# Optimization experiments

Measured on AMD Instinct MI355X. Metric: run time of the kernel, lower is better.

## Reference

```python
import jax, jax.numpy as jnp
import numpy as np

D_MODEL = 1024
N_HEAD = 16
D_HEAD = D_MODEL // N_HEAD
N_EXPERTS = 8
TOP_K = 2
D_FF = 4096
EPS = 1e-6


def setup_inputs() -> dict:
    key = jax.random.key(0)
    ks = jax.random.split(key, 16)
    s = 0.02  # init scale
    d, dff, E = D_MODEL, D_FF, N_EXPERTS
    return {
        "dec": jax.random.normal(ks[0], (4, 1024, d), jnp.float32),
        "text_encoder": jax.random.normal(ks[1], (4, 512, d), jnp.float32),
        # self-attention projections
        "Wq1": jax.random.normal(ks[2], (d, d), jnp.float32) * s,
        "Wk1": jax.random.normal(ks[3], (d, d), jnp.float32) * s,
        "Wv1": jax.random.normal(ks[4], (d, d), jnp.float32) * s,
        "Wo1": jax.random.normal(ks[5], (d, d), jnp.float32) * s,
        # cross-attention projections
        "Wq2": jax.random.normal(ks[6], (d, d), jnp.float32) * s,
        "Wk2": jax.random.normal(ks[7], (d, d), jnp.float32) * s,
        "Wv2": jax.random.normal(ks[8], (d, d), jnp.float32) * s,
        "Wo2": jax.random.normal(ks[9], (d, d), jnp.float32) * s,
        # shared RMSNorm gain (module uses one norm instance three times)
        "g": jnp.ones((d,), jnp.float32),
        # MoE router + per-expert FFN weights
        "Wg": jax.random.normal(ks[10], (d, E), jnp.float32) * s,
        "W1": jax.random.normal(ks[11], (E, d, dff), jnp.float32) * s,
        "W2": jax.random.normal(ks[12], (E, dff, d), jnp.float32) * s,
    }


def rmsnorm(x, g):
    return x * jax.lax.rsqrt(jnp.mean(x * x, axis=-1, keepdims=True) + EPS) * g


def mha(q_in, k_in, v_in, Wq, Wk, Wv, Wo):
    B, Sq, _ = q_in.shape
    Sk = k_in.shape[1]
    q = (q_in @ Wq).reshape(B, Sq, N_HEAD, D_HEAD)
    k = (k_in @ Wk).reshape(B, Sk, N_HEAD, D_HEAD)
    v = (v_in @ Wv).reshape(B, Sk, N_HEAD, D_HEAD)
    scores = jnp.einsum("bqhd,bkhd->bhqk", q, k) / jnp.sqrt(jnp.asarray(D_HEAD, q.dtype))
    attn = jax.nn.softmax(scores, axis=-1)
    out = jnp.einsum("bhqk,bkhd->bqhd", attn, v).reshape(B, Sq, D_MODEL)
    return out @ Wo


def moe(x, Wg, W1, W2):
    # top-k softmax router, renormalized weights; dense per-expert FFN with combine
    probs = jax.nn.softmax(x @ Wg, axis=-1)              # [B,S,E]
    weights, indices = jax.lax.top_k(probs, TOP_K)        # [B,S,k]
    weights = weights / jnp.sum(weights, axis=-1, keepdims=True)
    # combine[t,e] = sum_k weights[t,k] * (indices[t,k]==e)
    combine = jnp.sum(
        jax.nn.one_hot(indices, N_EXPERTS, dtype=x.dtype) * weights[..., None], axis=-2
    )  # [B,S,E]
    out = jnp.zeros_like(x)
    for e in range(N_EXPERTS):  # fixed small expert loop
        h = jax.nn.relu(x @ W1[e]) @ W2[e]
        out = out + combine[..., e:e + 1] * h
    return weights, indices, out


def reference(dec, text_encoder, Wq1, Wk1, Wv1, Wo1, Wq2, Wk2, Wv2, Wo2, g, Wg, W1, W2):
    # self-attention + residual + RMSNorm (dropout p=0 -> identity)
    x = rmsnorm(mha(dec, dec, dec, Wq1, Wk1, Wv1, Wo1) + dec, g)
    # cross-attention + residual + RMSNorm
    x = rmsnorm(mha(x, text_encoder, text_encoder, Wq2, Wk2, Wv2, Wo2) + x, g)
    # MoE FFN + residual + RMSNorm
    weights, indices, y = moe(x, Wg, W1, W2)
    x = rmsnorm(y + x, g)
    return weights, indices, x
```

## Files before the change

kernel.cpp:

```cpp
#include <hip/hip_runtime.h>
#include <stdint.h>

#define D_    1024
#define BB    4
#define SDEC  1024
#define STXT  512
#define TDEC  4096
#define TTXT  2048
#define NH    16
#define DHD   64
#define NE    8
#define DFF   4096
#define NSLOT 8192
#define ND1   8192
#define ND2   4096
#define MOEGRID 512

using u16 = unsigned short;
typedef __attribute__((ext_vector_type(8))) short bf16x8;
typedef __attribute__((ext_vector_type(4))) float f32x4;

__device__ __forceinline__ float bf2f(u16 h) {
    union { unsigned int u; float f; } x; x.u = ((unsigned int)h) << 16; return x.f;
}
__device__ __forceinline__ u16 f2bf(float f) {
    union { float f; unsigned int u; } x; x.f = f;
    unsigned int lsb = (x.u >> 16) & 1u;
    return (u16)((x.u + 0x7fffu + lsb) >> 16);
}

__device__ __forceinline__ void gld16(const u16* g, u16* l) {
    __builtin_amdgcn_global_load_lds((const __attribute__((address_space(1))) void*)g,
                                     (__attribute__((address_space(3))) void*)l,
                                     16, 0, 0);
}

constexpr int BM = 128, BK = 32;

template<int SPLIT, int EPI, int BROWS>
__global__ __launch_bounds__(256) void gemm_bt(
    const u16* __restrict__ AH, const u16* __restrict__ AL,
    const u16* __restrict__ BH, const u16* __restrict__ BL,
    float* __restrict__ Cf, u16* __restrict__ CH, u16* __restrict__ CL,
    int M, int N, int K, int lda, int ldb, int ldc, int nb2,
    long strA1, long strA2, long strB1, long strB2, long strC1, long strC2)
{
    constexpr int WM = (BROWS == 64) ? 2 : 4;
    constexpr int ASZ = BM * BK, BSZ = BROWS * BK;
    __shared__ u16 smem[(SPLIT ? 2 : 1) * (ASZ + BSZ)];
    u16* sAH = smem;
    u16* sBH = smem + ASZ;
    u16* sAL = SPLIT ? smem + ASZ + BSZ : nullptr;
    u16* sBL = SPLIT ? smem + 2 * ASZ + BSZ : nullptr;

    const int z = blockIdx.z;
    const int z1 = z / nb2, z2 = z % nb2;
    const long zA = (long)z1 * strA1 + (long)z2 * strA2;
    const long zB = (long)z1 * strB1 + (long)z2 * strB2;
    const long zC = (long)z1 * strC1 + (long)z2 * strC2;

    const int tileM = blockIdx.y * BM, tileN = blockIdx.x * BROWS;
    const int t = threadIdx.x;
    const int sr = t >> 2;
    const int sc = (t & 3) << 3;
    const u16* pA = AH + zA + (long)(tileM + sr) * lda + sc;
    const u16* pB = BH + zB + (long)(tileN + sr) * ldb + sc;
    const u16* pAl = nullptr; const u16* pBl = nullptr;
    if constexpr (SPLIT) {
        pAl = AL + zA + (long)(tileM + sr) * lda + sc;
        pBl = BL + zB + (long)(tileN + sr) * ldb + sc;
    }
    const long hA = 64L * lda, hB = 64L * ldb;

    const int lane = t & 63;
    const int wv = t >> 6;
    const int wr = (BROWS == 64) ? (wv << 5) : ((wv >> 1) << 6);
    const int wc = (BROWS == 64) ? 0 : ((wv & 1) << 6);
    const int fr = lane & 15, kg = lane >> 4;

    f32x4 acc[WM][4];
    const f32x4 vzero = {0.f, 0.f, 0.f, 0.f};
#pragma unroll
    for (int m = 0; m < WM; ++m)
#pragma unroll
        for (int n = 0; n < 4; ++n) acc[m][n] = vzero;

    for (int k0 = 0; k0 < K; k0 += BK) {
        gld16(pA + k0,      sAH + t * 8);
        gld16(pA + k0 + hA, sAH + 2048 + t * 8);
        gld16(pB + k0,      sBH + t * 8);
        if constexpr (BROWS == 128) gld16(pB + k0 + hB, sBH + 2048 + t * 8);
        if constexpr (SPLIT) {
            gld16(pAl + k0,      sAL + t * 8);
            gld16(pAl + k0 + hA, sAL + 2048 + t * 8);
            gld16(pBl + k0,      sBL + t * 8);
            if constexpr (BROWS == 128) gld16(pBl + k0 + hB, sBL + 2048 + t * 8);
        }
        __syncthreads();

        bf16x8 fa[WM], fb[4], fal[WM], fbl[4];
#pragma unroll
        for (int m = 0; m < WM; ++m) {
            fa[m] = *(const bf16x8*)&sAH[(wr + m * 16 + fr) * BK + (kg << 3)];
            if constexpr (SPLIT) fal[m] = *(const bf16x8*)&sAL[(wr + m * 16 + fr) * BK + (kg << 3)];
        }
#pragma unroll
        for (int n = 0; n < 4; ++n) {
            fb[n] = *(const bf16x8*)&sBH[(wc + n * 16 + fr) * BK + (kg << 3)];
            if constexpr (SPLIT) fbl[n] = *(const bf16x8*)&sBL[(wc + n * 16 + fr) * BK + (kg << 3)];
        }
#pragma unroll
        for (int m = 0; m < WM; ++m)
#pragma unroll
            for (int n = 0; n < 4; ++n) {
                acc[m][n] = __builtin_amdgcn_mfma_f32_16x16x32_bf16(fa[m], fb[n], acc[m][n], 0, 0, 0);
                if constexpr (SPLIT) {
                    acc[m][n] = __builtin_amdgcn_mfma_f32_16x16x32_bf16(fa[m],  fbl[n], acc[m][n], 0, 0, 0);
                    acc[m][n] = __builtin_amdgcn_mfma_f32_16x16x32_bf16(fal[m], fb[n],  acc[m][n], 0, 0, 0);
                }
            }
        __syncthreads();
    }

#pragma unroll
    for (int m = 0; m < WM; ++m) {
        const int r0 = tileM + wr + m * 16 + (kg << 2);
#pragma unroll
        for (int n = 0; n < 4; ++n) {
            const int col = tileN + wc + n * 16 + fr;
            if (col >= N) continue;
#pragma unroll
            for (int i = 0; i < 4; ++i) {
                const int r = r0 + i;
                if (r >= M) continue;
                const float v = acc[m][n][i];
                const long off = zC + (long)r * ldc + col;
                if constexpr (EPI == 0) {
                    Cf[off] = v;
                } else if constexpr (EPI == 1) {
                    const u16 h = f2bf(v);
                    CH[off] = h;
                    CL[off] = f2bf(v - bf2f(h));
                } else {
                    CH[off] = f2bf(fmaxf(v, 0.f));
                }
            }
        }
    }
}

__global__ __launch_bounds__(256) void scores_k64(
    const u16* __restrict__ AH, const u16* __restrict__ AL,
    const u16* __restrict__ BH, const u16* __restrict__ BL,
    u16* __restrict__ CH, u16* __restrict__ CL,
    int lda, int ldb, int ldc, int nb2,
    long strA1, long strA2, long strB1, long strB2, long strC1, long strC2)
{
    __shared__ u16 smem[4 * 8192];
    u16* sAH = smem;
    u16* sAL = smem + 8192;
    u16* sBH = smem + 16384;
    u16* sBL = smem + 24576;

    const int z = blockIdx.z;
    const int z1 = z / nb2, z2 = z % nb2;
    const long zA = (long)z1 * strA1 + (long)z2 * strA2;
    const long zB = (long)z1 * strB1 + (long)z2 * strB2;
    const long zC = (long)z1 * strC1 + (long)z2 * strC2;

    const int tileM = blockIdx.y * 128, tileN = blockIdx.x * 128;
    const int t = threadIdx.x;
    const int srow = t >> 3;
    const int scol = ((t & 7) ^ (srow & 7)) << 3;
    const u16* pA  = AH + zA + (long)(tileM + srow) * lda + scol;
    const u16* pAl = AL + zA + (long)(tileM + srow) * lda + scol;
    const u16* pB  = BH + zB + (long)(tileN + srow) * ldb + scol;
    const u16* pBl = BL + zB + (long)(tileN + srow) * ldb + scol;

#pragma unroll
    for (int c = 0; c < 4; ++c) {
        const long ro = 32L * c * lda;
        const long rb = 32L * c * ldb;
        gld16(pA  + ro, sAH + c * 2048 + t * 8);
        gld16(pAl + ro, sAL + c * 2048 + t * 8);
        gld16(pB  + rb, sBH + c * 2048 + t * 8);
        gld16(pBl + rb, sBL + c * 2048 + t * 8);
    }
    __syncthreads();

    const int lane = t & 63;
    const int wv = t >> 6;
    const int wr = (wv >> 1) << 6, wc = (wv & 1) << 6;
    const int fr = lane & 15, kg = lane >> 4;

    f32x4 acc[4][4];
    const f32x4 vzero = {0.f, 0.f, 0.f, 0.f};
#pragma unroll
    for (int m = 0; m < 4; ++m)
#pragma unroll
        for (int n = 0; n < 4; ++n) acc[m][n] = vzero;

#pragma unroll
    for (int ks = 0; ks < 2; ++ks) {
        bf16x8 fa[4], fb[4], fal[4], fbl[4];
#pragma unroll
        for (int m = 0; m < 4; ++m) {
            const int r = wr + m * 16 + fr;
            const int o = r * 64 + (((kg | (ks << 2)) ^ (r & 7)) << 3);
            fa[m]  = *(const bf16x8*)&sAH[o];
            fal[m] = *(const bf16x8*)&sAL[o];
        }
#pragma unroll
        for (int n = 0; n < 4; ++n) {
            const int r = wc + n * 16 + fr;
            const int o = r * 64 + (((kg | (ks << 2)) ^ (r & 7)) << 3);
            fb[n]  = *(const bf16x8*)&sBH[o];
            fbl[n] = *(const bf16x8*)&sBL[o];
        }
#pragma unroll
        for (int m = 0; m < 4; ++m)
#pragma unroll
            for (int n = 0; n < 4; ++n) {
                acc[m][n] = __builtin_amdgcn_mfma_f32_16x16x32_bf16(fa[m],  fb[n],  acc[m][n], 0, 0, 0);
                acc[m][n] = __builtin_amdgcn_mfma_f32_16x16x32_bf16(fa[m],  fbl[n], acc[m][n], 0, 0, 0);
                acc[m][n] = __builtin_amdgcn_mfma_f32_16x16x32_bf16(fal[m], fb[n],  acc[m][n], 0, 0, 0);
            }
    }

#pragma unroll
    for (int m = 0; m < 4; ++m) {
        const int r0 = tileM + wr + m * 16 + (kg << 2);
#pragma unroll
        for (int n = 0; n < 4; ++n) {
            const int col = tileN + wc + n * 16 + fr;
#pragma unroll
            for (int i = 0; i < 4; ++i) {
                const float v = acc[m][n][i];
                const long off = zC + (long)(r0 + i) * ldc + col;
                const u16 h = f2bf(v);
                CH[off] = h;
                CL[off] = f2bf(v - bf2f(h));
            }
        }
    }
}

__global__ __launch_bounds__(256) void pv_k64(
    const u16* __restrict__ PHp, const u16* __restrict__ PLp,
    const u16* __restrict__ VTH, const u16* __restrict__ VTL,
    float* __restrict__ Op, int Skv, int NZ)
{
    __shared__ u16 smem[24576];
    u16* sAH = smem;
    u16* sAL = smem + 8192;
    u16* sBH = smem + 16384;
    u16* sBL = smem + 20480;

    const int kq = blockIdx.x;
    const int tileM = blockIdx.y * 128;
    const int z = blockIdx.z;
    const int kbase = kq * (Skv >> 2);
    const int nrounds = Skv >> 8;

    const int t = threadIdx.x;
    const int srow = t >> 3;
    const int scol = ((t & 7) ^ (srow & 7)) << 3;
    const u16* pA  = PHp + (long)z * 1024 * Skv + (long)(tileM + srow) * Skv + kbase + scol;
    const u16* pAl = PLp + (long)z * 1024 * Skv + (long)(tileM + srow) * Skv + kbase + scol;
    const u16* pB  = VTH + (long)z * 64 * Skv + (long)srow * Skv + kbase + scol;
    const u16* pBl = VTL + (long)z * 64 * Skv + (long)srow * Skv + kbase + scol;

    const int lane = t & 63, wv = t >> 6;
    const int wr = wv << 5;
    const int fr = lane & 15, kg = lane >> 4;

    f32x4 acc[2][4];
    const f32x4 vzero = {0.f, 0.f, 0.f, 0.f};
#pragma unroll
    for (int m = 0; m < 2; ++m)
#pragma unroll
        for (int n = 0; n < 4; ++n) acc[m][n] = vzero;

    for (int rr = 0; rr < nrounds; ++rr) {
        const long k0 = (long)rr << 6;
#pragma unroll
        for (int c = 0; c < 4; ++c) {
            const long ro = 32L * c * Skv;
            gld16(pA  + k0 + ro, sAH + c * 2048 + t * 8);
            gld16(pAl + k0 + ro, sAL + c * 2048 + t * 8);
        }
#pragma unroll
        for (int c = 0; c < 2; ++c) {
            const long ro = 32L * c * Skv;
            gld16(pB  + k0 + ro, sBH + c * 2048 + t * 8);
            gld16(pBl + k0 + ro, sBL + c * 2048 + t * 8);
        }
        __syncthreads();

#pragma unroll
        for (int ks = 0; ks < 2; ++ks) {
            bf16x8 fa[2], fb[4], fal[2], fbl[4];
#pragma unroll
            for (int m = 0; m < 2; ++m) {
                const int r = wr + m * 16 + fr;
                const int o = r * 64 + (((kg | (ks << 2)) ^ (r & 7)) << 3);
                fa[m]  = *(const bf16x8*)&sAH[o];
                fal[m] = *(const bf16x8*)&sAL[o];
            }
#pragma unroll
            for (int n = 0; n < 4; ++n) {
                const int r = n * 16 + fr;
                const int o = r * 64 + (((kg | (ks << 2)) ^ (r & 7)) << 3);
                fb[n]  = *(const bf16x8*)&sBH[o];
                fbl[n] = *(const bf16x8*)&sBL[o];
            }
#pragma unroll
            for (int m = 0; m < 2; ++m)
#pragma unroll
                for (int n = 0; n < 4; ++n) {
                    acc[m][n] = __builtin_amdgcn_mfma_f32_16x16x32_bf16(fa[m],  fb[n],  acc[m][n], 0, 0, 0);
                    acc[m][n] = __builtin_amdgcn_mfma_f32_16x16x32_bf16(fa[m],  fbl[n], acc[m][n], 0, 0, 0);
                    acc[m][n] = __builtin_amdgcn_mfma_f32_16x16x32_bf16(fal[m], fb[n],  acc[m][n], 0, 0, 0);
                }
        }
        __syncthreads();
    }

    const long base = ((long)kq * NZ + z) * 65536;
#pragma unroll
    for (int m = 0; m < 2; ++m) {
        const int r0 = tileM + wr + m * 16 + (kg << 2);
#pragma unroll
        for (int n = 0; n < 4; ++n) {
            const int col = n * 16 + fr;
#pragma unroll
            for (int i = 0; i < 4; ++i)
                Op[base + (long)(r0 + i) * 64 + col] = acc[m][n][i];
        }
    }
}

__global__ __launch_bounds__(256) void pv_combine(
    const float* __restrict__ Op, u16* __restrict__ aoH, u16* __restrict__ aoL,
    int nz, int nh)
{
    const long i = ((long)blockIdx.x * 256 + threadIdx.x) * 4;
    const int zz = (int)(i >> 16);
    const int rem = (int)(i & 65535);
    const int r = rem >> 6, c = rem & 63;
    const int b = zz / nh, h = zz % nh;
    const long kqS = (long)nz * 65536;
    float4 v = *(const float4*)(Op + i);
    const float4 v1 = *(const float4*)(Op + kqS + i);
    const float4 v2 = *(const float4*)(Op + 2 * kqS + i);
    const float4 v3 = *(const float4*)(Op + 3 * kqS + i);
    v.x += v1.x + v2.x + v3.x;
    v.y += v1.y + v2.y + v3.y;
    v.z += v1.z + v2.z + v3.z;
    v.w += v1.w + v2.w + v3.w;
    const long dst = (long)b * SDEC * D_ + (long)r * D_ + h * 64 + c;
    u16 h0 = f2bf(v.x), h1 = f2bf(v.y), h2 = f2bf(v.z), h3 = f2bf(v.w);
    uint2 hh;
    hh.x = (unsigned)h0 | ((unsigned)h1 << 16);
    hh.y = (unsigned)h2 | ((unsigned)h3 << 16);
    *(uint2*)(aoH + dst) = hh;
    u16 l0 = f2bf(v.x - bf2f(h0)), l1 = f2bf(v.y - bf2f(h1));
    u16 l2 = f2bf(v.z - bf2f(h2)), l3 = f2bf(v.w - bf2f(h3));
    uint2 ll;
    ll.x = (unsigned)l0 | ((unsigned)l1 << 16);
    ll.y = (unsigned)l2 | ((unsigned)l3 << 16);
    *(uint2*)(aoL + dst) = ll;
}

template<int EPI>
__global__ __launch_bounds__(256, 2) void moe_gemm2(
    const u16* __restrict__ Ag, int lda,
    const u16* __restrict__ BTbase, int ldb, long btStride,
    float* __restrict__ Cf0, float* __restrict__ Cf1, u16* __restrict__ CH, int ldc,
    const int4* __restrict__ desc, int ndesc, int Kiter)
{
    __shared__ u16 smem[32768];
    const int t = threadIdx.x;
    const int lane = t & 63, wv = t >> 6;
    const int wr = (wv >> 1) << 6, wc = (wv & 1) << 6;
    const int fr = lane & 15, kg = lane >> 4;
    const int nks = Kiter >> 5;

    const int rS = t >> 2;
    const int cS = ((t & 3) ^ ((t >> 3) & 3)) << 3;

    int ldsA[4], ldsB[4];
#pragma unroll
    for (int m = 0; m < 4; ++m) {
        const int ra = wr + m * 16 + fr;
        ldsA[m] = ra * 32 + ((kg ^ ((ra >> 1) & 3)) << 3);
        const int rb = wc + m * 16 + fr;
        ldsB[m] = rb * 32 + ((kg ^ ((rb >> 1) & 3)) << 3);
    }

    for (int p = blockIdx.x; p < ndesc; p += MOEGRID) {
        const int4 d = desc[p];
        if (d.x < 0) continue;
        const int rowbase = d.x, colbase = d.y & 0xFFFF, e = d.y >> 16;
        const int kbase = d.z, s1 = d.w;
        const u16* paS = Ag + (long)(rowbase + rS) * lda + kbase + cS;
        const u16* pbS = BTbase + (long)e * btStride + (long)(colbase + rS) * ldb + kbase + cS;
        const long hA = 64L * lda, hB = 64L * ldb;

        f32x4 acc[4][4];
        const f32x4 vzero = {0.f, 0.f, 0.f, 0.f};
#pragma unroll
        for (int m = 0; m < 4; ++m)
#pragma unroll
            for (int n = 0; n < 4; ++n) acc[m][n] = vzero;

#define STG(ks) { const int s_ = (ks) & 3; const long k0_ = (long)(ks) << 5; \
        u16* b_ = smem + s_ * 8192; \
        gld16(paS + k0_,      b_ + t * 8); \
        gld16(paS + k0_ + hA, b_ + 2048 + t * 8); \
        gld16(pbS + k0_,      b_ + 4096 + t * 8); \
        gld16(pbS + k0_ + hB, b_ + 6144 + t * 8); }

        STG(0); STG(1); STG(2);
        asm volatile("s_waitcnt vmcnt(8)" ::: "memory");
        __builtin_amdgcn_s_barrier();
        __builtin_amdgcn_sched_barrier(0);

        for (int ks = 0; ks < nks; ++ks) {
            if (ks + 3 < nks) STG(ks + 3);
            const u16* sA = smem + (ks & 3) * 8192;
            const u16* sB = sA + 4096;
            bf16x8 fa[4], fb[4];
#pragma unroll
            for (int m = 0; m < 4; ++m) fa[m] = *(const bf16x8*)&sA[ldsA[m]];
#pragma unroll
            for (int n = 0; n < 4; ++n) fb[n] = *(const bf16x8*)&sB[ldsB[n]];
            __builtin_amdgcn_s_setprio(1);
#pragma unroll
            for (int m = 0; m < 4; ++m)
#pragma unroll
                for (int n = 0; n < 4; ++n)
                    acc[m][n] = __builtin_amdgcn_mfma_f32_16x16x32_bf16(fa[m], fb[n], acc[m][n], 0, 0, 0);
            __builtin_amdgcn_s_setprio(0);
            if (ks + 3 < nks)      { asm volatile("s_waitcnt vmcnt(8)" ::: "memory"); }
            else if (ks + 2 < nks) { asm volatile("s_waitcnt vmcnt(4)" ::: "memory"); }
            else                   { asm volatile("s_waitcnt vmcnt(0)" ::: "memory"); }
            __builtin_amdgcn_s_barrier();
            __builtin_amdgcn_sched_barrier(0);
        }
#undef STG

        float* __restrict__ C = (EPI == 0) ? ((kbase == 0) ? Cf0 : Cf1) : nullptr;
#pragma unroll
        for (int m = 0; m < 4; ++m) {
            const int r0 = rowbase + wr + m * 16 + (kg << 2);
#pragma unroll
            for (int n = 0; n < 4; ++n) {
                const int col = colbase + wc + n * 16 + fr;
#pragma unroll
                for (int i = 0; i < 4; ++i) {
                    const int r = r0 + i;
                    if (r >= s1) continue;
                    const float v = acc[m][n][i];
                    const long off = (long)r * ldc + col;
                    if constexpr (EPI == 0) C[off] = v;
                    else                    CH[off] = f2bf(fmaxf(v, 0.f));
                }
            }
        }
    }
}

__global__ __launch_bounds__(256) void split2k(const float* __restrict__ in,
                                               u16* __restrict__ oh, u16* __restrict__ ol, long n)
{
    long i = ((long)blockIdx.x * 256 + threadIdx.x) * 4;
    if (i >= n) return;
    float4 v = *(const float4*)(in + i);
    u16 h0 = f2bf(v.x), h1 = f2bf(v.y), h2 = f2bf(v.z), h3 = f2bf(v.w);
    uint2 oo;
    oo.x = (unsigned)h0 | ((unsigned)h1 << 16);
    oo.y = (unsigned)h2 | ((unsigned)h3 << 16);
    *(uint2*)(oh + i) = oo;
    if (ol) {
        u16 l0 = f2bf(v.x - bf2f(h0)), l1 = f2bf(v.y - bf2f(h1));
        u16 l2 = f2bf(v.z - bf2f(h2)), l3 = f2bf(v.w - bf2f(h3));
        uint2 ll;
        ll.x = (unsigned)l0 | ((unsigned)l1 << 16);
        ll.y = (unsigned)l2 | ((unsigned)l3 << 16);
        *(uint2*)(ol + i) = ll;
    }
}

struct Ptr8 { const float* p[8]; };
__global__ __launch_bounds__(256) void transpose_split_w(
    Ptr8 in, u16* __restrict__ oh, u16* __restrict__ ol)
{
    __shared__ float tile[32][33];
    const int z = blockIdx.z;
    const float* ip = in.p[z];
    u16* ohp = oh + (long)z * D_ * D_;
    u16* olp = ol + (long)z * D_ * D_;
    const int c0 = blockIdx.x * 32, r0 = blockIdx.y * 32;
    const int tx = threadIdx.x & 31, ty = threadIdx.x >> 5;
    for (int i = ty; i < 32; i += 8)
        tile[i][tx] = ip[(long)(r0 + i) * D_ + c0 + tx];
    __syncthreads();
    for (int i = ty; i < 32; i += 8) {
        int oc = c0 + i, orr = r0 + tx;
        float v = tile[tx][i];
        u16 h = f2bf(v);
        ohp[(long)oc * D_ + orr] = h;
        olp[(long)oc * D_ + orr] = f2bf(v - bf2f(h));
    }
}

__global__ __launch_bounds__(256) void transpose_split(
    const float* __restrict__ in, u16* __restrict__ oh, u16* __restrict__ ol,
    int R, int C, int ild, long ibs1, long ibs2, int nb2, int old_, long obs)
{
    __shared__ float tile[32][33];
    const int z = blockIdx.z;
    const float* ip = in + (long)(z / nb2) * ibs1 + (long)(z % nb2) * ibs2;
    u16* ohp = oh + (long)z * obs;
    u16* olp = ol ? ol + (long)z * obs : nullptr;
    const int c0 = blockIdx.x * 32, r0 = blockIdx.y * 32;
    const int tx = threadIdx.x & 31, ty = threadIdx.x >> 5;
    for (int i = ty; i < 32; i += 8) {
        int r = r0 + i, c = c0 + tx;
        tile[i][tx] = (r < R && c < C) ? ip[(long)r * ild + c] : 0.f;
    }
    __syncthreads();
    for (int i = ty; i < 32; i += 8) {
        int oc = c0 + i, orr = r0 + tx;
        if (oc < C && orr < R) {
            float v = tile[tx][i];
            u16 h = f2bf(v);
            ohp[(long)oc * old_ + orr] = h;
            if (olp) olp[(long)oc * old_ + orr] = f2bf(v - bf2f(h));
        }
    }
}

__global__ __launch_bounds__(256) void transpose_split_hl(
    const u16* __restrict__ inH, const u16* __restrict__ inL,
    u16* __restrict__ oh, u16* __restrict__ ol,
    int R, int C, int ild, long ibs1, long ibs2, int nb2, int old_, long obs)
{
    __shared__ float tile[32][33];
    const int z = blockIdx.z;
    const long base = (long)(z / nb2) * ibs1 + (long)(z % nb2) * ibs2;
    u16* ohp = oh + (long)z * obs;
    u16* olp = ol + (long)z * obs;
    const int c0 = blockIdx.x * 32, r0 = blockIdx.y * 32;
    const int tx = threadIdx.x & 31, ty = threadIdx.x >> 5;
    for (int i = ty; i < 32; i += 8) {
        int r = r0 + i, c = c0 + tx;
        float v = 0.f;
        if (r < R && c < C) {
            const long o = base + (long)r * ild + c;
            v = bf2f(inH[o]) + bf2f(inL[o]);
        }
        tile[i][tx] = v;
    }
    __syncthreads();
    for (int i = ty; i < 32; i += 8) {
        int oc = c0 + i, orr = r0 + tx;
        if (oc < C && orr < R) {
            float v = tile[tx][i];
            u16 h = f2bf(v);
            ohp[(long)oc * old_ + orr] = h;
            olp[(long)oc * old_ + orr] = f2bf(v - bf2f(h));
        }
    }
}

__global__ __launch_bounds__(256) void softmax_hl(
    u16* __restrict__ ph, u16* __restrict__ pl, int cols, float scale)
{
    u16* php = ph + (long)blockIdx.x * cols;
    u16* plp = pl + (long)blockIdx.x * cols;
    const int t = threadIdx.x;
    float v[4];
    int vpt;
    if (cols == 1024) {
        vpt = 4;
        uint2 hh = ((const uint2*)php)[t];
        uint2 ll = ((const uint2*)plp)[t];
        v[0] = (bf2f((u16)(hh.x & 0xffff)) + bf2f((u16)(ll.x & 0xffff))) * scale;
        v[1] = (bf2f((u16)(hh.x >> 16))    + bf2f((u16)(ll.x >> 16)))    * scale;
        v[2] = (bf2f((u16)(hh.y & 0xffff)) + bf2f((u16)(ll.y & 0xffff))) * scale;
        v[3] = (bf2f((u16)(hh.y >> 16))    + bf2f((u16)(ll.y >> 16)))    * scale;
    } else {
        vpt = 2;
        unsigned hh = ((const unsigned*)php)[t];
        unsigned ll = ((const unsigned*)plp)[t];
        v[0] = (bf2f((u16)(hh & 0xffff)) + bf2f((u16)(ll & 0xffff))) * scale;
        v[1] = (bf2f((u16)(hh >> 16))    + bf2f((u16)(ll >> 16)))    * scale;
        v[2] = -3.4e38f; v[3] = -3.4e38f;
    }
    float mx = fmaxf(fmaxf(v[0], v[1]), fmaxf(v[2], v[3]));
#pragma unroll
    for (int o = 32; o; o >>= 1) mx = fmaxf(mx, __shfl_xor(mx, o));
    __shared__ float sm[4];
    const int wv = t >> 6, ln = t & 63;
    if (ln == 0) sm[wv] = mx;
    __syncthreads();
    mx = fmaxf(fmaxf(sm[0], sm[1]), fmaxf(sm[2], sm[3]));
    float sum = 0.f;
    for (int i = 0; i < vpt; ++i) { v[i] = expf(v[i] - mx); sum += v[i]; }
#pragma unroll
    for (int o = 32; o; o >>= 1) sum += __shfl_xor(sum, o);
    __shared__ float ss[4];
    if (ln == 0) ss[wv] = sum;
    __syncthreads();
    sum = ss[0] + ss[1] + ss[2] + ss[3];
    const float inv = 1.f / sum;
    if (cols == 1024) {
        float q0 = v[0] * inv, q1 = v[1] * inv, q2 = v[2] * inv, q3 = v[3] * inv;
        u16 h0 = f2bf(q0), h1 = f2bf(q1), h2 = f2bf(q2), h3 = f2bf(q3);
        uint2 hh; hh.x = (unsigned)h0 | ((unsigned)h1 << 16); hh.y = (unsigned)h2 | ((unsigned)h3 << 16);
        ((uint2*)php)[t] = hh;
        u16 l0 = f2bf(q0 - bf2f(h0)), l1 = f2bf(q1 - bf2f(h1));
        u16 l2 = f2bf(q2 - bf2f(h2)), l3 = f2bf(q3 - bf2f(h3));
        uint2 llo; llo.x = (unsigned)l0 | ((unsigned)l1 << 16); llo.y = (unsigned)l2 | ((unsigned)l3 << 16);
        ((uint2*)plp)[t] = llo;
    } else {
        float q0 = v[0] * inv, q1 = v[1] * inv;
        u16 h0 = f2bf(q0), h1 = f2bf(q1);
        ((unsigned*)php)[t] = (unsigned)h0 | ((unsigned)h1 << 16);
        u16 l0 = f2bf(q0 - bf2f(h0)), l1 = f2bf(q1 - bf2f(h1));
        ((unsigned*)plp)[t] = (unsigned)l0 | ((unsigned)l1 << 16);
    }
}

__global__ __launch_bounds__(256) void add_rmsnorm(
    const float* __restrict__ a, const float* __restrict__ b, const float* __restrict__ g,
    float* __restrict__ xo, u16* __restrict__ xh, u16* __restrict__ xl)
{
    const long row = blockIdx.x;
    const int t = threadIdx.x;
    const float* pa = a + row * D_;
    const float* pb = b + row * D_;
    float v[4]; double ssq = 0.0;
#pragma unroll
    for (int i = 0; i < 4; ++i) {
        int c = t + (i << 8);
        v[i] = pa[c] + pb[c];
        ssq += (double)v[i] * v[i];
    }
#pragma unroll
    for (int o = 32; o; o >>= 1) ssq += __shfl_xor(ssq, o);
    __shared__ double sd[4];
    if ((t & 63) == 0) sd[t >> 6] = ssq;
    __syncthreads();
    ssq = sd[0] + sd[1] + sd[2] + sd[3];
    const float rs = (float)(1.0 / sqrt(ssq * (1.0 / 1024.0) + 1e-6));
#pragma unroll
    for (int i = 0; i < 4; ++i) {
        int c = t + (i << 8);
        float o = v[i] * rs * g[c];
        xo[row * D_ + c] = o;
        if (xh) {
            u16 h = f2bf(o);
            xh[row * D_ + c] = h;
            if (xl) xl[row * D_ + c] = f2bf(o - bf2f(h));
        }
    }
}

__global__ __launch_bounds__(256) void router_topk(
    const float* __restrict__ x2, const float* __restrict__ Wg,
    float* __restrict__ outw, float* __restrict__ outi,
    int* __restrict__ idx, float* __restrict__ tokw, int* __restrict__ counts, int T)
{
    const int wid = (int)((blockIdx.x * 256 + threadIdx.x) >> 6);
    const int lane = threadIdx.x & 63;
    if (wid >= T) return;
    float acc[NE];
#pragma unroll
    for (int e = 0; e < NE; ++e) acc[e] = 0.f;
    const float* xr = x2 + (long)wid * D_;
    for (int i = 0; i < 16; ++i) {
        float xv = xr[i * 64 + lane];
        const float* wr = Wg + (long)(i * 64 + lane) * NE;
#pragma unroll
        for (int e = 0; e < NE; ++e) acc[e] += xv * wr[e];
    }
#pragma unroll
    for (int e = 0; e < NE; ++e)
#pragma unroll
        for (int o = 32; o; o >>= 1) acc[e] += __shfl_xor(acc[e], o);
    if (lane == 0) {
        float m = acc[0];
#pragma unroll
        for (int e = 1; e < NE; ++e) m = fmaxf(m, acc[e]);
        float p[NE], s = 0.f;
#pragma unroll
        for (int e = 0; e < NE; ++e) { p[e] = expf(acc[e] - m); s += p[e]; }
        const float invs = 1.f / s;
#pragma unroll
        for (int e = 0; e < NE; ++e) p[e] *= invs;
        int e0 = 0;
#pragma unroll
        for (int e = 1; e < NE; ++e) if (p[e] > p[e0]) e0 = e;
        int e1 = (e0 == 0) ? 1 : 0;
#pragma unroll
        for (int e = 0; e < NE; ++e) if (e != e0 && e != e1 && p[e] > p[e1]) e1 = e;
        float w0 = p[e0], w1 = p[e1];
        const float sw = 1.f / (w0 + w1);
        w0 *= sw; w1 *= sw;
        outw[2 * wid] = w0;      outw[2 * wid + 1] = w1;
        outi[2 * wid] = (float)e0; outi[2 * wid + 1] = (float)e1;
        idx[2 * wid] = e0;       idx[2 * wid + 1] = e1;
        tokw[2 * wid] = w0;      tokw[2 * wid + 1] = w1;
        atomicAdd(&counts[e0], 1);
        atomicAdd(&counts[e1], 1);
    }
}

__global__ void scan_desc(const int* __restrict__ counts, int* __restrict__ cursor,
                          int4* __restrict__ d1, int4* __restrict__ d2)
{
    __shared__ int sseg[NE + 1];
    if (threadIdx.x == 0) {
        int a = 0;
        for (int e = 0; e < NE; ++e) { sseg[e] = a; cursor[e] = a; a += counts[e]; }
        sseg[NE] = a;
    }
    __syncthreads();
    const int e = threadIdx.x;
    if (e < NE) {
        const int s0 = sseg[e], s1 = sseg[e + 1];
        const int nyt = (s1 - s0 + 127) >> 7;
        for (int xt = 0; xt < 32; ++xt)
            for (int yt = 0; yt < nyt; ++yt)
                d1[e + 8 * (xt * nyt + yt)] =
                    make_int4(s0 + yt * 128, (xt * 128) | (e << 16), 0, s1);
        for (int kh = 0; kh < 2; ++kh)
            for (int xt = 0; xt < 8; ++xt)
                for (int yt = 0; yt < nyt; ++yt)
                    d2[e + 8 * ((kh * 8 + xt) * nyt + yt)] =
                        make_int4(s0 + yt * 128, (xt * 128) | (e << 16), kh * 2048, s1);
    }
}

__global__ __launch_bounds__(256) void scatter_slots(
    const int* __restrict__ idx, int* __restrict__ cursor,
    int* __restrict__ row_token, int* __restrict__ slot_of, int T)
{
    const int t = blockIdx.x * 256 + threadIdx.x;
    if (t >= T) return;
#pragma unroll
    for (int k = 0; k < 2; ++k) {
        const int e = idx[2 * t + k];
        const int pos = atomicAdd(&cursor[e], 1);
        row_token[pos] = t;
        slot_of[2 * t + k] = pos;
    }
}

__global__ __launch_bounds__(256) void gather_bf16(
    const float* __restrict__ x2, const int* __restrict__ row_token, u16* __restrict__ Xg)
{
    const int r = blockIdx.x;
    const int t = threadIdx.x;
    const float* src = x2 + (long)row_token[r] * D_ + t * 4;
    float4 v = *(const float4*)src;
    uint2 oo;
    oo.x = (unsigned)f2bf(v.x) | ((unsigned)f2bf(v.y) << 16);
    oo.y = (unsigned)f2bf(v.z) | ((unsigned)f2bf(v.w) << 16);
    *(uint2*)(Xg + (long)r * D_ + t * 4) = oo;
}

__global__ __launch_bounds__(256) void combine_rmsnorm(
    const float* __restrict__ Y0, const float* __restrict__ Y1,
    const int* __restrict__ slot_of, const float* __restrict__ tokw,
    const float* __restrict__ x2, const float* __restrict__ g, float* __restrict__ out)
{
    const long tr = blockIdx.x;
    const int t = threadIdx.x;
    const int s0 = slot_of[2 * tr], s1 = slot_of[2 * tr + 1];
    const float w0 = tokw[2 * tr], w1 = tokw[2 * tr + 1];
    const float* ya0 = Y0 + (long)s0 * D_;
    const float* yb0 = Y1 + (long)s0 * D_;
    const float* ya1 = Y0 + (long)s1 * D_;
    const float* yb1 = Y1 + (long)s1 * D_;
    const float* xr = x2 + tr * D_;
    float v[4]; double ssq = 0.0;
#pragma unroll
    for (int i = 0; i < 4; ++i) {
        int c = t + (i << 8);
        v[i] = w0 * (ya0[c] + yb0[c]) + w1 * (ya1[c] + yb1[c]) + xr[c];
        ssq += (double)v[i] * v[i];
    }
#pragma unroll
    for (int o = 32; o; o >>= 1) ssq += __shfl_xor(ssq, o);
    __shared__ double sd[4];
    if ((t & 63) == 0) sd[t >> 6] = ssq;
    __syncthreads();
    ssq = sd[0] + sd[1] + sd[2] + sd[3];
    const float rs = (float)(1.0 / sqrt(ssq * (1.0 / 1024.0) + 1e-6));
#pragma unroll
    for (int i = 0; i < 4; ++i) {
        int c = t + (i << 8);
        out[tr * D_ + c] = v[i] * rs * g[c];
    }
}

__global__ void sentinel(float* o) { o[0] = 12345.0f; }

extern "C" void kernel_launch(void* const* d_in, const int* in_sizes, int n_in,
                              void* d_out, int out_size, void* d_ws, size_t ws_size,
                              hipStream_t stream)
{
    const float* dec = (const float*)d_in[0];
    const float* te  = (const float*)d_in[1];
    const float* g  = (const float*)d_in[10];
    const float* Wg = (const float*)d_in[11];
    const float* W1 = (const float*)d_in[12];
    const float* W2 = (const float*)d_in[13];
    float* outw = (float*)d_out;
    float* outi = outw + 2 * TDEC;
    float* outx = outw + 4 * TDEC;

    char* ws = (char*)d_ws;
    size_t off = 0;
    auto A = [&](size_t bytes) -> char* {
        char* p = ws + off;
        off += (bytes + 255) & ~(size_t)255;
        return p;
    };

    u16* decH = (u16*)A((size_t)TDEC * D_ * 2);
    u16* decL = (u16*)A((size_t)TDEC * D_ * 2);
    u16* teH  = (u16*)A((size_t)TTXT * D_ * 2);
    u16* teL  = (u16*)A((size_t)TTXT * D_ * 2);
    u16* wtHall = (u16*)A((size_t)8 * D_ * D_ * 2);
    u16* wtLall = (u16*)A((size_t)8 * D_ * D_ * 2);
    float* x1f = (float*)A((size_t)TDEC * D_ * 4);
    float* x2f = (float*)A((size_t)TDEC * D_ * 4);
    float* tokw = (float*)A(NSLOT * 4);
    int* idx    = (int*)A(NSLOT * 4);
    int* counts = (int*)A(256);
    int* cursor = (int*)A(256);
    int* row_token = (int*)A(NSLOT * 4);
    int* slot_of   = (int*)A(NSLOT * 4);
    int4* desc1 = (int4*)A((size_t)ND1 * 16);
    int4* desc2 = (int4*)A((size_t)ND2 * 16);
    const size_t Rbase = off;

    u16* W1T  = (u16*)A((size_t)NE * DFF * D_ * 2);
    u16* W2T  = (u16*)A((size_t)NE * D_ * DFF * 2);
    u16* Xg   = (u16*)A((size_t)(NSLOT + 256) * D_ * 2);
    u16* Hb   = (u16*)A((size_t)(NSLOT + 256) * DFF * 2);
    float* Yseg = (float*)A((size_t)NSLOT * D_ * 4);
    float* Ypart1 = (float*)W1T;
    const size_t moeEnd = off;

    auto allocAttn = [&](bool batched, u16*& PH, u16*& PL, u16*& qkvH, u16*& qkvL,
                         u16*& q2H, u16*& q2L, u16*& kv2H, u16*& kv2L,
                         u16*& vTH, u16*& vTL, u16*& aoH, u16*& aoL,
                         u16*& x1H, u16*& x1L, float*& of, float*& Opart) {
        off = Rbase;
        const size_t pcell = batched ? (size_t)BB * NH * SDEC * SDEC * 2
                                     : (size_t)NH * SDEC * SDEC * 2;
        PH = (u16*)A(pcell);
        PL = (u16*)A(pcell);
        qkvH = (u16*)A((size_t)TDEC * 3 * D_ * 2);
        qkvL = (u16*)A((size_t)TDEC * 3 * D_ * 2);
        q2H  = (u16*)A((size_t)TDEC * D_ * 2);
        q2L  = (u16*)A((size_t)TDEC * D_ * 2);
        kv2H = (u16*)A((size_t)TTXT * 2 * D_ * 2);
        kv2L = (u16*)A((size_t)TTXT * 2 * D_ * 2);
        vTH = (u16*)A((size_t)TDEC * D_ * 2);
        vTL = (u16*)A((size_t)TDEC * D_ * 2);
        aoH = (u16*)A((size_t)TDEC * D_ * 2);
        aoL = (u16*)A((size_t)TDEC * D_ * 2);
        x1H = (u16*)A((size_t)TDEC * D_ * 2);
        x1L = (u16*)A((size_t)TDEC * D_ * 2);
        of  = (float*)A((size_t)TDEC * D_ * 4);
        Opart = (float*)A((size_t)4 * (batched ? BB * NH : NH) * SDEC * DHD * 4);
        return off;
    };

    u16 *PH, *PL, *qkvH, *qkvL, *q2H, *q2L, *kv2H, *kv2L, *vTH, *vTL, *aoH, *aoL, *x1H, *x1L;
    float *of, *Opart;
    size_t attnEnd = allocAttn(true, PH, PL, qkvH, qkvL, q2H, q2L, kv2H, kv2L,
                               vTH, vTL, aoH, aoL, x1H, x1L, of, Opart);
    bool batched = ws_size >= (attnEnd > moeEnd ? attnEnd : moeEnd);
    if (!batched) {
        attnEnd = allocAttn(false, PH, PL, qkvH, qkvL, q2H, q2L, kv2H, kv2L,
                            vTH, vTL, aoH, aoL, x1H, x1L, of, Opart);
        if (ws_size < (attnEnd > moeEnd ? attnEnd : moeEnd)) {
            sentinel<<<1, 1, 0, stream>>>(outw);
            return;
        }
    }

    const dim3 blk(256);

    split2k<<<dim3((TDEC * D_) / 1024), blk, 0, stream>>>(dec, decH, decL, (long)TDEC * D_);
    split2k<<<dim3((TTXT * D_) / 1024), blk, 0, stream>>>(te, teH, teL, (long)TTXT * D_);
    Ptr8 wp;
    for (int i = 0; i < 8; ++i) wp.p[i] = (const float*)d_in[2 + i];
    transpose_split_w<<<dim3(32, 32, 8), blk, 0, stream>>>(wp, wtHall, wtLall);

    gemm_bt<1, 1, 64><<<dim3(48, 32, 1), blk, 0, stream>>>(decH, decL, wtHall, wtLall,
        nullptr, qkvH, qkvL, TDEC, 3 * D_, D_, D_, D_, 3 * D_, 1, 0, 0, 0, 0, 0, 0);
    transpose_split_hl<<<dim3(2, 32, BB * NH), blk, 0, stream>>>(qkvH + 2 * D_, qkvL + 2 * D_,
        vTH, vTL, SDEC, DHD, 3 * D_, (long)SDEC * 3 * D_, DHD, NH, SDEC, (long)DHD * SDEC);

    if (batched) {
        scores_k64<<<dim3(8, 8, BB * NH), blk, 0, stream>>>(
            qkvH, qkvL, qkvH + D_, qkvL + D_, PH, PL,
            3 * D_, 3 * D_, SDEC, NH,
            (long)SDEC * 3 * D_, DHD, (long)SDEC * 3 * D_, DHD,
            (long)NH * SDEC * SDEC, (long)SDEC * SDEC);
        softmax_hl<<<dim3(BB * NH * SDEC), blk, 0, stream>>>(PH, PL, SDEC, 0.125f);
        pv_k64<<<dim3(4, 8, BB * NH), blk, 0, stream>>>(PH, PL, vTH, vTL, Opart, SDEC, BB * NH);
        pv_combine<<<dim3(BB * NH * 64), blk, 0, stream>>>(Opart, aoH, aoL, BB * NH, NH);
    } else {
        for (int b = 0; b < BB; ++b) {
            const long qo3 = (long)b * SDEC * 3 * D_;
            const long qo  = (long)b * SDEC * D_;
            scores_k64<<<dim3(8, 8, NH), blk, 0, stream>>>(
                qkvH + qo3, qkvL + qo3, qkvH + qo3 + D_, qkvL + qo3 + D_,
                PH, PL, 3 * D_, 3 * D_, SDEC, NH,
                0, DHD, 0, DHD, 0, (long)SDEC * SDEC);
            softmax_hl<<<dim3(NH * SDEC), blk, 0, stream>>>(PH, PL, SDEC, 0.125f);
            pv_k64<<<dim3(4, 8, NH), blk, 0, stream>>>(PH, PL,
                vTH + (long)b * NH * DHD * SDEC, vTL + (long)b * NH * DHD * SDEC,
                Opart, SDEC, NH);
            pv_combine<<<dim3(NH * 64), blk, 0, stream>>>(Opart, aoH + qo, aoL + qo, NH, NH);
        }
    }
    gemm_bt<1, 0, 64><<<dim3(16, 32, 1), blk, 0, stream>>>(aoH, aoL,
        wtHall + (size_t)3 * D_ * D_, wtLall + (size_t)3 * D_ * D_,
        of, nullptr, nullptr, TDEC, D_, D_, D_, D_, D_, 1, 0, 0, 0, 0, 0, 0);
    add_rmsnorm<<<dim3(TDEC), blk, 0, stream>>>(of, dec, g, x1f, x1H, x1L);

    gemm_bt<1, 1, 64><<<dim3(16, 32, 1), blk, 0, stream>>>(x1H, x1L,
        wtHall + (size_t)4 * D_ * D_, wtLall + (size_t)4 * D_ * D_,
        nullptr, q2H, q2L, TDEC, D_, D_, D_, D_, D_, 1, 0, 0, 0, 0, 0, 0);
    gemm_bt<1, 1, 64><<<dim3(32, 16, 1), blk, 0, stream>>>(teH, teL,
        wtHall + (size_t)5 * D_ * D_, wtLall + (size_t)5 * D_ * D_,
        nullptr, kv2H, kv2L, TTXT, 2 * D_, D_, D_, D_, 2 * D_, 1, 0, 0, 0, 0, 0, 0);
    transpose_split_hl<<<dim3(2, 16, BB * NH), blk, 0, stream>>>(kv2H + D_, kv2L + D_,
        vTH, vTL, STXT, DHD, 2 * D_, (long)STXT * 2 * D_, DHD, NH, STXT, (long)DHD * STXT);

    if (batched) {
        scores_k64<<<dim3(4, 8, BB * NH), blk, 0, stream>>>(
            q2H, q2L, kv2H, kv2L, PH, PL,
            D_, 2 * D_, STXT, NH,
            (long)SDEC * D_, DHD, (long)STXT * 2 * D_, DHD,
            (long)NH * SDEC * STXT, (long)SDEC * STXT);
        softmax_hl<<<dim3(BB * NH * SDEC), blk, 0, stream>>>(PH, PL, STXT, 0.125f);
        pv_k64<<<dim3(4, 8, BB * NH), blk, 0, stream>>>(PH, PL, vTH, vTL, Opart, STXT, BB * NH);
        pv_combine<<<dim3(BB * NH * 64), blk, 0, stream>>>(Opart, aoH, aoL, BB * NH, NH);
    } else {
        for (int b = 0; b < BB; ++b) {
            const long qo  = (long)b * SDEC * D_;
            const long ko2 = (long)b * STXT * 2 * D_;
            scores_k64<<<dim3(4, 8, NH), blk, 0, stream>>>(
                q2H + qo, q2L + qo, kv2H + ko2, kv2L + ko2,
                PH, PL, D_, 2 * D_, STXT, NH,
                0, DHD, 0, DHD, 0, (long)SDEC * STXT);
            softmax_hl<<<dim3(NH * SDEC), blk, 0, stream>>>(PH, PL, STXT, 0.125f);
            pv_k64<<<dim3(4, 8, NH), blk, 0, stream>>>(PH, PL,
                vTH + (long)b * NH * DHD * STXT, vTL + (long)b * NH * DHD * STXT,
                Opart, STXT, NH);
            pv_combine<<<dim3(NH * 64), blk, 0, stream>>>(Opart, aoH + qo, aoL + qo, NH, NH);
        }
    }
    gemm_bt<1, 0, 64><<<dim3(16, 32, 1), blk, 0, stream>>>(aoH, aoL,
        wtHall + (size_t)7 * D_ * D_, wtLall + (size_t)7 * D_ * D_,
        of, nullptr, nullptr, TDEC, D_, D_, D_, D_, D_, 1, 0, 0, 0, 0, 0, 0);
    add_rmsnorm<<<dim3(TDEC), blk, 0, stream>>>(of, x1f, g, x2f, nullptr, nullptr);

    hipMemsetAsync(counts, 0, 32, stream);
    hipMemsetAsync(desc1, 0xFF, (size_t)ND1 * 16, stream);
    hipMemsetAsync(desc2, 0xFF, (size_t)ND2 * 16, stream);
    router_topk<<<dim3(TDEC / 4), blk, 0, stream>>>(x2f, Wg, outw, outi, idx, tokw, counts, TDEC);
    scan_desc<<<1, 64, 0, stream>>>(counts, cursor, desc1, desc2);
    scatter_slots<<<dim3(TDEC / 256), blk, 0, stream>>>(idx, cursor, row_token, slot_of, TDEC);
    gather_bf16<<<dim3(NSLOT), blk, 0, stream>>>(x2f, row_token, Xg);

    transpose_split<<<dim3(DFF / 32, D_ / 32, NE), blk, 0, stream>>>(W1, W1T, nullptr,
        D_, DFF, DFF, (long)D_ * DFF, 0, 1, D_, (long)DFF * D_);
    transpose_split<<<dim3(D_ / 32, DFF / 32, NE), blk, 0, stream>>>(W2, W2T, nullptr,
        DFF, D_, D_, (long)D_ * DFF, 0, 1, DFF, (long)D_ * DFF);
    moe_gemm2<2><<<dim3(MOEGRID), blk, 0, stream>>>(Xg, D_, W1T, D_, (long)DFF * D_,
        nullptr, nullptr, Hb, DFF, desc1, ND1, 1024);
    moe_gemm2<0><<<dim3(MOEGRID), blk, 0, stream>>>(Hb, DFF, W2T, DFF, (long)D_ * DFF,
        Yseg, Ypart1, nullptr, D_, desc2, ND2, 2048);
    combine_rmsnorm<<<dim3(TDEC), blk, 0, stream>>>(Yseg, Ypart1, slot_of, tokw, x2f, g, outx);

    (void)in_sizes; (void)n_in; (void)out_size;
}
```

Before: 1.299 ms.

## Fuse softmax normalization into PV kernel using precomputed row statistics

Replaces the in-place softmax pass with a row-statistics kernel that only reads scores and writes per-row max and inverse sum. The PV kernel then reads raw scores, applies exp and normalization in registers, splits to hi/lo bf16 and stores to shared memory before the MFMAs. This removes the write-back of the full probability matrix. In exchange, the A-tile load moves from asynchronous global-to-LDS copies to register loads with extra exp arithmetic inside the PV loop.

```diff
diff --git a/kernel.cpp b/kernel.cpp
--- a/kernel.cpp
+++ b/kernel.cpp
@@ -245,14 +245,61 @@
     }
 }
 
-__global__ __launch_bounds__(256) void pv_k64(
-    const u16* __restrict__ PHp, const u16* __restrict__ PLp,
+__global__ __launch_bounds__(256) void rowstat(
+    const u16* __restrict__ sh, const u16* __restrict__ sl,
+    float2* __restrict__ stats, int cols, float scale)
+{
+    const u16* shp = sh + (long)blockIdx.x * cols;
+    const u16* slp = sl + (long)blockIdx.x * cols;
+    const int t = threadIdx.x;
+    float v[4];
+    int vpt;
+    if (cols == 1024) {
+        vpt = 4;
+        uint2 hh = ((const uint2*)shp)[t];
+        uint2 ll = ((const uint2*)slp)[t];
+        v[0] = (bf2f((u16)(hh.x & 0xffff)) + bf2f((u16)(ll.x & 0xffff))) * scale;
+        v[1] = (bf2f((u16)(hh.x >> 16))    + bf2f((u16)(ll.x >> 16)))    * scale;
+        v[2] = (bf2f((u16)(hh.y & 0xffff)) + bf2f((u16)(ll.y & 0xffff))) * scale;
+        v[3] = (bf2f((u16)(hh.y >> 16))    + bf2f((u16)(ll.y >> 16)))    * scale;
+    } else {
+        vpt = 2;
+        unsigned hh = ((const unsigned*)shp)[t];
+        unsigned ll = ((const unsigned*)slp)[t];
+        v[0] = (bf2f((u16)(hh & 0xffff)) + bf2f((u16)(ll & 0xffff))) * scale;
+        v[1] = (bf2f((u16)(hh >> 16))    + bf2f((u16)(ll >> 16)))    * scale;
+        v[2] = -3.4e38f; v[3] = -3.4e38f;
+    }
+    float mx = fmaxf(fmaxf(v[0], v[1]), fmaxf(v[2], v[3]));
+#pragma unroll
+    for (int o = 32; o; o >>= 1) mx = fmaxf(mx, __shfl_xor(mx, o));
+    __shared__ float sm[4];
+    const int wv = t >> 6, ln = t & 63;
+    if (ln == 0) sm[wv] = mx;
+    __syncthreads();
+    mx = fmaxf(fmaxf(sm[0], sm[1]), fmaxf(sm[2], sm[3]));
+    float sum = 0.f;
+    for (int i = 0; i < vpt; ++i) sum += expf(v[i] - mx);
+#pragma unroll
+    for (int o = 32; o; o >>= 1) sum += __shfl_xor(sum, o);
+    __shared__ float ss[4];
+    if (ln == 0) ss[wv] = sum;
+    __syncthreads();
+    if (t == 0) {
+        sum = ss[0] + ss[1] + ss[2] + ss[3];
+        stats[blockIdx.x] = make_float2(mx, 1.f / sum);
+    }
+}
+
+__global__ __launch_bounds__(256) void pv_k64_sm(
+    const u16* __restrict__ SH, const u16* __restrict__ SL,
+    const float2* __restrict__ stats,
     const u16* __restrict__ VTH, const u16* __restrict__ VTL,
-    float* __restrict__ Op, int Skv, int NZ)
+    float* __restrict__ Op, int Skv, int NZ, float scale)
 {
     __shared__ u16 smem[24576];
-    u16* sAH = smem;
-    u16* sAL = smem + 8192;
+    u16* sPH = smem;
+    u16* sPL = smem + 8192;
     u16* sBH = smem + 16384;
     u16* sBL = smem + 20480;
 
@@ -263,12 +310,17 @@
     const int nrounds = Skv >> 8;
 
     const int t = threadIdx.x;
-    const int srow = t >> 3;
-    const int scol = ((t & 7) ^ (srow & 7)) << 3;
-    const u16* pA  = PHp + (long)z * 1024 * Skv + (long)(tileM + srow) * Skv + kbase + scol;
-    const u16* pAl = PLp + (long)z * 1024 * Skv + (long)(tileM + srow) * Skv + kbase + scol;
-    const u16* pB  = VTH + (long)z * 64 * Skv + (long)srow * Skv + kbase + scol;
-    const u16* pBl = VTL + (long)z * 64 * Skv + (long)srow * Skv + kbase + scol;
+    const int arow = t >> 3;
+    const int achk = t & 7;
+    const u16* pSH = SH + (long)z * 1024 * Skv + (long)(tileM + arow) * Skv + kbase + (achk << 3);
+    const u16* pSL = SL + (long)z * 1024 * Skv + (long)(tileM + arow) * Skv + kbase + (achk << 3);
+    float2 st[4];
+#pragma unroll
+    for (int c = 0; c < 4; ++c) st[c] = stats[(long)z * 1024 + tileM + arow + 32 * c];
+
+    const int scol = (achk ^ (arow & 7)) << 3;
+    const u16* pB  = VTH + (long)z * 64 * Skv + (long)arow * Skv + kbase + scol;
+    const u16* pBl = VTL + (long)z * 64 * Skv + (long)arow * Skv + kbase + scol;
 
     const int lane = t & 63, wv = t >> 6;
     const int wr = wv << 5;
@@ -283,18 +335,36 @@
 
     for (int rr = 0; rr < nrounds; ++rr) {
         const long k0 = (long)rr << 6;
-#pragma unroll
-        for (int c = 0; c < 4; ++c) {
-            const long ro = 32L * c * Skv;
-            gld16(pA  + k0 + ro, sAH + c * 2048 + t * 8);
-            gld16(pAl + k0 + ro, sAL + c * 2048 + t * 8);
-        }
 #pragma unroll
         for (int c = 0; c < 2; ++c) {
             const long ro = 32L * c * Skv;
             gld16(pB  + k0 + ro, sBH + c * 2048 + t * 8);
             gld16(pBl + k0 + ro, sBL + c * 2048 + t * 8);
         }
+#pragma unroll
+        for (int c = 0; c < 4; ++c) {
+            const long ro = 32L * c * Skv;
+            const uint4 hv = *(const uint4*)(pSH + k0 + ro);
+            const uint4 lv = *(const uint4*)(pSL + k0 + ro);
+            const float m_ = st[c].x, inv_ = st[c].y;
+            const unsigned hw[4] = {hv.x, hv.y, hv.z, hv.w};
+            const unsigned lw[4] = {lv.x, lv.y, lv.z, lv.w};
+            unsigned ph[4], pl[4];
+#pragma unroll
+            for (int j = 0; j < 4; ++j) {
+                const float s0 = bf2f((u16)(hw[j] & 0xffff)) + bf2f((u16)(lw[j] & 0xffff));
+                const float s1 = bf2f((u16)(hw[j] >> 16))    + bf2f((u16)(lw[j] >> 16));
+                const float p0 = expf(fmaf(s0, scale, -m_)) * inv_;
+                const float p1 = expf(fmaf(s1, scale, -m_)) * inv_;
+                const u16 h0 = f2bf(p0), h1 = f2bf(p1);
+                ph[j] = (unsigned)h0 | ((unsigned)h1 << 16);
+                pl[j] = (unsigned)f2bf(p0 - bf2f(h0)) | ((unsigned)f2bf(p1 - bf2f(h1)) << 16);
+            }
+            const int r = arow + 32 * c;
+            const int dst = r * 64 + ((achk ^ (r & 7)) << 3);
+            *(uint4*)&sPH[dst] = make_uint4(ph[0], ph[1], ph[2], ph[3]);
+            *(uint4*)&sPL[dst] = make_uint4(pl[0], pl[1], pl[2], pl[3]);
+        }
         __syncthreads();
 
 #pragma unroll
@@ -304,8 +374,8 @@
             for (int m = 0; m < 2; ++m) {
                 const int r = wr + m * 16 + fr;
                 const int o = r * 64 + (((kg | (ks << 2)) ^ (r & 7)) << 3);
-                fa[m]  = *(const bf16x8*)&sAH[o];
-                fal[m] = *(const bf16x8*)&sAL[o];
+                fa[m]  = *(const bf16x8*)&sPH[o];
+                fal[m] = *(const bf16x8*)&sPL[o];
             }
 #pragma unroll
             for (int n = 0; n < 4; ++n) {
@@ -575,65 +645,6 @@
     }
 }
 
-__global__ __launch_bounds__(256) void softmax_hl(
-    u16* __restrict__ ph, u16* __restrict__ pl, int cols, float scale)
-{
-    u16* php = ph + (long)blockIdx.x * cols;
-    u16* plp = pl + (long)blockIdx.x * cols;
-    const int t = threadIdx.x;
-    float v[4];
-    int vpt;
-    if (cols == 1024) {
-        vpt = 4;
-        uint2 hh = ((const uint2*)php)[t];
-        uint2 ll = ((const uint2*)plp)[t];
-        v[0] = (bf2f((u16)(hh.x & 0xffff)) + bf2f((u16)(ll.x & 0xffff))) * scale;
-        v[1] = (bf2f((u16)(hh.x >> 16))    + bf2f((u16)(ll.x >> 16)))    * scale;
-        v[2] = (bf2f((u16)(hh.y & 0xffff)) + bf2f((u16)(ll.y & 0xffff))) * scale;
-        v[3] = (bf2f((u16)(hh.y >> 16))    + bf2f((u16)(ll.y >> 16)))    * scale;
-    } else {
-        vpt = 2;
-        unsigned hh = ((const unsigned*)php)[t];
-        unsigned ll = ((const unsigned*)plp)[t];
-        v[0] = (bf2f((u16)(hh & 0xffff)) + bf2f((u16)(ll & 0xffff))) * scale;
-        v[1] = (bf2f((u16)(hh >> 16))    + bf2f((u16)(ll >> 16)))    * scale;
-        v[2] = -3.4e38f; v[3] = -3.4e38f;
-    }
-    float mx = fmaxf(fmaxf(v[0], v[1]), fmaxf(v[2], v[3]));
-#pragma unroll
-    for (int o = 32; o; o >>= 1) mx = fmaxf(mx, __shfl_xor(mx, o));
-    __shared__ float sm[4];
-    const int wv = t >> 6, ln = t & 63;
-    if (ln == 0) sm[wv] = mx;
-    __syncthreads();
-    mx = fmaxf(fmaxf(sm[0], sm[1]), fmaxf(sm[2], sm[3]));
-    float sum = 0.f;
-    for (int i = 0; i < vpt; ++i) { v[i] = expf(v[i] - mx); sum += v[i]; }
-#pragma unroll
-    for (int o = 32; o; o >>= 1) sum += __shfl_xor(sum, o);
-    __shared__ float ss[4];
-    if (ln == 0) ss[wv] = sum;
-    __syncthreads();
-    sum = ss[0] + ss[1] + ss[2] + ss[3];
-    const float inv = 1.f / sum;
-    if (cols == 1024) {
-        float q0 = v[0] * inv, q1 = v[1] * inv, q2 = v[2] * inv, q3 = v[3] * inv;
-        u16 h0 = f2bf(q0), h1 = f2bf(q1), h2 = f2bf(q2), h3 = f2bf(q3);
-        uint2 hh; hh.x = (unsigned)h0 | ((unsigned)h1 << 16); hh.y = (unsigned)h2 | ((unsigned)h3 << 16);
-        ((uint2*)php)[t] = hh;
-        u16 l0 = f2bf(q0 - bf2f(h0)), l1 = f2bf(q1 - bf2f(h1));
-        u16 l2 = f2bf(q2 - bf2f(h2)), l3 = f2bf(q3 - bf2f(h3));
-        uint2 llo; llo.x = (unsigned)l0 | ((unsigned)l1 << 16); llo.y = (unsigned)l2 | ((unsigned)l3 << 16);
-        ((uint2*)plp)[t] = llo;
-    } else {
-        float q0 = v[0] * inv, q1 = v[1] * inv;
-        u16 h0 = f2bf(q0), h1 = f2bf(q1);
-        ((unsigned*)php)[t] = (unsigned)h0 | ((unsigned)h1 << 16);
-        u16 l0 = f2bf(q0 - bf2f(h0)), l1 = f2bf(q1 - bf2f(h1));
-        ((unsigned*)plp)[t] = (unsigned)l0 | ((unsigned)l1 << 16);
-    }
-}
-
 __global__ __launch_bounds__(256) void add_rmsnorm(
     const float* __restrict__ a, const float* __restrict__ b, const float* __restrict__ g,
     float* __restrict__ xo, u16* __restrict__ xh, u16* __restrict__ xl)
@@ -861,12 +872,11 @@
     auto allocAttn = [&](bool batched, u16*& PH, u16*& PL, u16*& qkvH, u16*& qkvL,
                          u16*& q2H, u16*& q2L, u16*& kv2H, u16*& kv2L,
                          u16*& vTH, u16*& vTL, u16*& aoH, u16*& aoL,
-                         u16*& x1H, u16*& x1L, float*& of, float*& Opart) {
+                         u16*& x1H, u16*& x1L, float*& of, float*& Opart, float2*& stats) {
         off = Rbase;
-        const size_t pcell = batched ? (size_t)BB * NH * SDEC * SDEC * 2
-                                     : (size_t)NH * SDEC * SDEC * 2;
-        PH = (u16*)A(pcell);
-        PL = (u16*)A(pcell);
+        const size_t nz = batched ? (size_t)BB * NH : (size_t)NH;
+        PH = (u16*)A(nz * SDEC * SDEC * 2);
+        PL = (u16*)A(nz * SDEC * SDEC * 2);
         qkvH = (u16*)A((size_t)TDEC * 3 * D_ * 2);
         qkvL = (u16*)A((size_t)TDEC * 3 * D_ * 2);
         q2H  = (u16*)A((size_t)TDEC * D_ * 2);
@@ -880,18 +890,20 @@
         x1H = (u16*)A((size_t)TDEC * D_ * 2);
         x1L = (u16*)A((size_t)TDEC * D_ * 2);
         of  = (float*)A((size_t)TDEC * D_ * 4);
-        Opart = (float*)A((size_t)4 * (batched ? BB * NH : NH) * SDEC * DHD * 4);
+        Opart = (float*)A((size_t)4 * nz * SDEC * DHD * 4);
+        stats = (float2*)A(nz * SDEC * 8);
         return off;
     };
 
     u16 *PH, *PL, *qkvH, *qkvL, *q2H, *q2L, *kv2H, *kv2L, *vTH, *vTL, *aoH, *aoL, *x1H, *x1L;
     float *of, *Opart;
+    float2* stats;
     size_t attnEnd = allocAttn(true, PH, PL, qkvH, qkvL, q2H, q2L, kv2H, kv2L,
-                               vTH, vTL, aoH, aoL, x1H, x1L, of, Opart);
+                               vTH, vTL, aoH, aoL, x1H, x1L, of, Opart, stats);
     bool batched = ws_size >= (attnEnd > moeEnd ? attnEnd : moeEnd);
     if (!batched) {
         attnEnd = allocAttn(false, PH, PL, qkvH, qkvL, q2H, q2L, kv2H, kv2L,
-                            vTH, vTL, aoH, aoL, x1H, x1L, of, Opart);
+                            vTH, vTL, aoH, aoL, x1H, x1L, of, Opart, stats);
         if (ws_size < (attnEnd > moeEnd ? attnEnd : moeEnd)) {
             sentinel<<<1, 1, 0, stream>>>(outw);
             return;
@@ -917,8 +929,9 @@
             3 * D_, 3 * D_, SDEC, NH,
             (long)SDEC * 3 * D_, DHD, (long)SDEC * 3 * D_, DHD,
             (long)NH * SDEC * SDEC, (long)SDEC * SDEC);
-        softmax_hl<<<dim3(BB * NH * SDEC), blk, 0, stream>>>(PH, PL, SDEC, 0.125f);
-        pv_k64<<<dim3(4, 8, BB * NH), blk, 0, stream>>>(PH, PL, vTH, vTL, Opart, SDEC, BB * NH);
+        rowstat<<<dim3(BB * NH * SDEC), blk, 0, stream>>>(PH, PL, (float2*)stats, SDEC, 0.125f);
+        pv_k64_sm<<<dim3(4, 8, BB * NH), blk, 0, stream>>>(PH, PL, stats, vTH, vTL,
+            Opart, SDEC, BB * NH, 0.125f);
         pv_combine<<<dim3(BB * NH * 64), blk, 0, stream>>>(Opart, aoH, aoL, BB * NH, NH);
     } else {
         for (int b = 0; b < BB; ++b) {
@@ -928,10 +941,10 @@
                 qkvH + qo3, qkvL + qo3, qkvH + qo3 + D_, qkvL + qo3 + D_,
                 PH, PL, 3 * D_, 3 * D_, SDEC, NH,
                 0, DHD, 0, DHD, 0, (long)SDEC * SDEC);
-            softmax_hl<<<dim3(NH * SDEC), blk, 0, stream>>>(PH, PL, SDEC, 0.125f);
-            pv_k64<<<dim3(4, 8, NH), blk, 0, stream>>>(PH, PL,
+            rowstat<<<dim3(NH * SDEC), blk, 0, stream>>>(PH, PL, stats, SDEC, 0.125f);
+            pv_k64_sm<<<dim3(4, 8, NH), blk, 0, stream>>>(PH, PL, stats,
                 vTH + (long)b * NH * DHD * SDEC, vTL + (long)b * NH * DHD * SDEC,
-                Opart, SDEC, NH);
+                Opart, SDEC, NH, 0.125f);
             pv_combine<<<dim3(NH * 64), blk, 0, stream>>>(Opart, aoH + qo, aoL + qo, NH, NH);
         }
     }
@@ -955,8 +968,9 @@
             D_, 2 * D_, STXT, NH,
             (long)SDEC * D_, DHD, (long)STXT * 2 * D_, DHD,
             (long)NH * SDEC * STXT, (long)SDEC * STXT);
-        softmax_hl<<<dim3(BB * NH * SDEC), blk, 0, stream>>>(PH, PL, STXT, 0.125f);
-        pv_k64<<<dim3(4, 8, BB * NH), blk, 0, stream>>>(PH, PL, vTH, vTL, Opart, STXT, BB * NH);
+        rowstat<<<dim3(BB * NH * SDEC), blk, 0, stream>>>(PH, PL, stats, STXT, 0.125f);
+        pv_k64_sm<<<dim3(4, 8, BB * NH), blk, 0, stream>>>(PH, PL, stats, vTH, vTL,
+            Opart, STXT, BB * NH, 0.125f);
         pv_combine<<<dim3(BB * NH * 64), blk, 0, stream>>>(Opart, aoH, aoL, BB * NH, NH);
     } else {
         for (int b = 0; b < BB; ++b) {
@@ -966,10 +980,10 @@
                 q2H + qo, q2L + qo, kv2H + ko2, kv2L + ko2,
                 PH, PL, D_, 2 * D_, STXT, NH,
                 0, DHD, 0, DHD, 0, (long)SDEC * STXT);
-            softmax_hl<<<dim3(NH * SDEC), blk, 0, stream>>>(PH, PL, STXT, 0.125f);
-            pv_k64<<<dim3(4, 8, NH), blk, 0, stream>>>(PH, PL,
+            rowstat<<<dim3(NH * SDEC), blk, 0, stream>>>(PH, PL, stats, STXT, 0.125f);
+            pv_k64_sm<<<dim3(4, 8, NH), blk, 0, stream>>>(PH, PL, stats,
                 vTH + (long)b * NH * DHD * STXT, vTL + (long)b * NH * DHD * STXT,
-                Opart, STXT, NH);
+                Opart, STXT, NH, 0.125f);
             pv_combine<<<dim3(NH * 64), blk, 0, stream>>>(Opart, aoH + qo, aoL + qo, NH, NH);
         }
     }
```

New measurement: 1.304 ms. No clear change (+0.4%).
